# Kernel tuning notes

Hardware: AMD Instinct MI355X
Metric: run time of the kernel (lower is better)

Reference implementation:

```python
import jax, jax.numpy as jnp
import numpy as np

W_LOSS = 10.0
THRESHOLD = 1.0
ACOS_EPS = 1e-7


def _normalize(v, eps=1e-8):
    n = jnp.linalg.norm(v, axis=-1, keepdims=True)
    return v / jnp.maximum(n, eps)


def quat_to_rotmat(q):
    # q: (..., 4) in (w, x, y, z) order, as in Zhou et al. / EPN repo
    q = _normalize(q)
    w, x, y, z = q[..., 0], q[..., 1], q[..., 2], q[..., 3]
    R = jnp.stack([
        1 - 2 * (y * y + z * z), 2 * (x * y - z * w), 2 * (x * z + y * w),
        2 * (x * y + z * w), 1 - 2 * (x * x + z * z), 2 * (y * z - x * w),
        2 * (x * z - y * w), 2 * (y * z + x * w), 1 - 2 * (x * x + y * y),
    ], axis=-1)
    return R.reshape(q.shape[:-1] + (3, 3))


def acos_safe(x):
    return jnp.arccos(jnp.clip(x, -1.0 + ACOS_EPS, 1.0 - ACOS_EPS))


def angle_from_R(R):
    # R: (..., 3, 3) -> geodesic angle via trace
    tr = jnp.trace(R, axis1=-2, axis2=-1)
    return acos_safe(0.5 * (tr - 1.0))


def setup_inputs() -> dict:
    key = jax.random.key(0)
    k1, k2, k3, k4, k5 = jax.random.split(key, 5)
    B, NA, NR = 32768, 60, 4
    wts = jax.random.normal(k1, (B, NA), dtype=jnp.float32)
    label = jax.random.randint(k2, (B,), 0, NA, dtype=jnp.int64)
    y = jax.random.normal(k3, (B, NR, NA), dtype=jnp.float32)
    # gt_R and anchors are valid rotation matrices (via random quaternions)
    gt_R = quat_to_rotmat(jax.random.normal(k4, (B, NA, 4), dtype=jnp.float32))
    anchors = quat_to_rotmat(jax.random.normal(k5, (NA, 4), dtype=jnp.float32))
    return {"wts": wts, "label": label, "y": y, "gt_R": gt_R, "anchors": anchors}


def reference(wts, label, y, gt_R, anchors):
    b, na = wts.shape
    nr = y.shape[1]
    true_R = gt_R[:, 29]  # (b, 3, 3)

    # --- CrossEntropyLoss branch (classifier) ---
    logp = jax.nn.log_softmax(wts, axis=1)
    cls_loss = -jnp.mean(jnp.take_along_axis(logp, label[:, None], axis=1))
    preds = jnp.argmax(wts, axis=1)  # (b,)
    r_acc = jnp.mean((preds == label).astype(jnp.float32))

    # --- anchor-wise predicted rotations ---
    # y (b, nr, na) -> (b, na, nr) -> (b, na, 3, 3)
    pred_RAnchor = quat_to_rotmat(jnp.swapaxes(y, 1, 2))

    gt_bias = angle_from_R(gt_R)  # (b, na)
    mask = (gt_bias < THRESHOLD).astype(gt_R.dtype)[:, :, None, None]
    l2_loss = jnp.sum(jnp.square(gt_R * mask - pred_RAnchor * mask))
    loss = cls_loss + W_LOSS * l2_loss

    # --- final predicted rotation: gather best anchor, compose with anchor rot ---
    sel = jnp.take_along_axis(pred_RAnchor, preds[:, None, None, None], axis=1)[:, 0]  # (b,3,3)
    pred_R = jnp.einsum('bij,bjk->bik', anchors[preds], sel)

    # --- mean angular error ---
    ang_err = angle_from_R(jnp.einsum('bij,bkj->bik', pred_R, true_R))  # (b,)

    return (loss, cls_loss, W_LOSS * l2_loss, r_acc, ang_err)
```

## Files before the change

kernel.cpp:

```cpp
#include <hip/hip_runtime.h>
#include <math.h>

constexpr int Bc  = 32768;
constexpr int NAc = 60;

constexpr int BPB  = 4;
constexpr int NBLK = Bc / BPB;
constexpr int ROWF = NAc * 9;
constexpr int STG4 = BPB * ROWF / 4;

#define COS_ONE 0.5403023058681398f

__global__ __launch_bounds__(256) void mtl_all(
    const float* __restrict__ wts,
    const int*   __restrict__ label,
    const float* __restrict__ y,
    const float* __restrict__ gt_R,
    const float* __restrict__ anchors,
    float*       __restrict__ out,
    float*       __restrict__ l2p,
    float*       __restrict__ lpp,
    float*       __restrict__ crp)
{
    __shared__ __align__(16) float sg[BPB * ROWF + 16];
    const int tid  = threadIdx.x;
    const int lane = tid & 63;
    const int wave = tid >> 6;
    const int b0   = blockIdx.x * BPB;
    const int b    = b0 + wave;

    const float4* gb4 = (const float4*)(gt_R + (size_t)b0 * ROWF);
    float4* sg4 = (float4*)sg;
    sg4[tid]       = gb4[tid];
    sg4[tid + 256] = gb4[tid + 256];
    if (tid < STG4 - 512) sg4[tid + 512] = gb4[tid + 512];

    const int a = lane;
    int lab = label[b];
    float w = -INFINITY;
    float qw = 0, qx = 0, qy = 0, qz = 0;
    float A0=0,A1=0,A2=0,A3=0,A4=0,A5=0,A6=0,A7=0,A8=0;
    if (a < NAc) {
        w = wts[(size_t)b * NAc + a];
        const float* yb = y + (size_t)b * (4 * NAc) + a;
        qw = yb[0 * NAc];
        qx = yb[1 * NAc];
        qy = yb[2 * NAc];
        qz = yb[3 * NAc];
        const float* Ar = anchors + a * 9;
        A0 = Ar[0]; A1 = Ar[1]; A2 = Ar[2];
        A3 = Ar[3]; A4 = Ar[4]; A5 = Ar[5];
        A6 = Ar[6]; A7 = Ar[7]; A8 = Ar[8];
    }

    float n   = sqrtf(qw*qw + qx*qx + qy*qy + qz*qz);
    float inv = 1.0f / fmaxf(n, 1e-8f);
    float pw = qw*inv, px = qx*inv, py = qy*inv, pz = qz*inv;
    float R00 = 1.0f - 2.0f*(py*py + pz*pz);
    float R01 = 2.0f*(px*py - pz*pw);
    float R02 = 2.0f*(px*pz + py*pw);
    float R10 = 2.0f*(px*py + pz*pw);
    float R11 = 1.0f - 2.0f*(px*px + pz*pz);
    float R12 = 2.0f*(py*pz - px*pw);
    float R20 = 2.0f*(px*pz - py*pw);
    float R21 = 2.0f*(py*pz + px*pw);
    float R22 = 1.0f - 2.0f*(px*px + py*py);

    __syncthreads();

    float acc = 0.0f;
    if (a < NAc) {
        const float* g = sg + wave * ROWF + a * 9;
        float g0 = g[0], g1 = g[1], g2 = g[2];
        float g3 = g[3], g4 = g[4], g5 = g[5];
        float g6 = g[6], g7 = g[7], g8 = g[8];
        float xb = 0.5f * (g0 + g4 + g8 - 1.0f);
        if (xb > COS_ONE) {
            float d0 = g0-R00, d1 = g1-R01, d2 = g2-R02;
            float d3 = g3-R10, d4 = g4-R11, d5 = g5-R12;
            float d6 = g6-R20, d7 = g7-R21, d8 = g8-R22;
            acc = d0*d0 + d1*d1 + d2*d2
                + d3*d3 + d4*d4 + d5*d5
                + d6*d6 + d7*d7 + d8*d8;
        }
    }

    float mv = w;
    int   mi = lane;
    for (int off = 32; off; off >>= 1) {
        float ov = __shfl_xor(mv, off, 64);
        int   oi = __shfl_xor(mi, off, 64);
        if (ov > mv || (ov == mv && oi < mi)) { mv = ov; mi = oi; }
    }
    float e  = (a < NAc) ? expf(w - mv) : 0.0f;
    float se = e;
    for (int off = 32; off; off >>= 1) se += __shfl_xor(se, off, 64);
    float lse  = mv + logf(se);
    float wlab = __shfl(w, lab, 64);

    if (lane == mi) {
        float P00 = A0*R00 + A1*R10 + A2*R20;
        float P01 = A0*R01 + A1*R11 + A2*R21;
        float P02 = A0*R02 + A1*R12 + A2*R22;
        float P10 = A3*R00 + A4*R10 + A5*R20;
        float P11 = A3*R01 + A4*R11 + A5*R21;
        float P12 = A3*R02 + A4*R12 + A5*R22;
        float P20 = A6*R00 + A7*R10 + A8*R20;
        float P21 = A6*R01 + A7*R11 + A8*R21;
        float P22 = A6*R02 + A7*R12 + A8*R22;
        const float* tR = sg + wave * ROWF + 29 * 9;
        float tr = P00*tR[0] + P01*tR[1] + P02*tR[2]
                 + P10*tR[3] + P11*tR[4] + P12*tR[5]
                 + P20*tR[6] + P21*tR[7] + P22*tR[8];
        float cx = 0.5f * (tr - 1.0f);
        cx = fminf(fmaxf(cx, -1.0f + 1e-7f), 1.0f - 1e-7f);
        out[4 + b] = acosf(cx);
    }

    for (int off = 32; off; off >>= 1) acc += __shfl_xor(acc, off, 64);

    float* s_l2 = sg + BPB * ROWF;
    float* s_lp = s_l2 + 4;
    float* s_cr = s_lp + 4;
    if (lane == 0) {
        s_l2[wave] = acc;
        s_lp[wave] = wlab - lse;
        s_cr[wave] = (mi == lab) ? 1.0f : 0.0f;
    }
    __syncthreads();
    if (tid == 0) {
        l2p[blockIdx.x] = s_l2[0] + s_l2[1] + s_l2[2] + s_l2[3];
        lpp[blockIdx.x] = s_lp[0] + s_lp[1] + s_lp[2] + s_lp[3];
        crp[blockIdx.x] = s_cr[0] + s_cr[1] + s_cr[2] + s_cr[3];
    }
}

__global__ __launch_bounds__(256) void mtl_final(
    const float* __restrict__ l2p,
    const float* __restrict__ lpp,
    const float* __restrict__ crp,
    float*       __restrict__ out)
{
    const int tid  = threadIdx.x;
    const int lane = tid & 63;
    const int wave = tid >> 6;

    double l2 = 0.0, lp = 0.0, cr = 0.0;
    const float4* l2p4 = (const float4*)l2p;
    const float4* lpp4 = (const float4*)lpp;
    const float4* crp4 = (const float4*)crp;
    for (int i = tid; i < NBLK / 4; i += 256) {
        float4 v = l2p4[i];
        l2 += (double)v.x + (double)v.y + (double)v.z + (double)v.w;
        float4 u = lpp4[i];
        lp += (double)u.x + (double)u.y + (double)u.z + (double)u.w;
        float4 c = crp4[i];
        cr += (double)c.x + (double)c.y + (double)c.z + (double)c.w;
    }

    for (int off = 32; off; off >>= 1) {
        l2 += __shfl_xor(l2, off, 64);
        lp += __shfl_xor(lp, off, 64);
        cr += __shfl_xor(cr, off, 64);
    }
    __shared__ double s_l2[4], s_lp[4], s_cr[4];
    if (lane == 0) { s_l2[wave] = l2; s_lp[wave] = lp; s_cr[wave] = cr; }
    __syncthreads();
    if (tid == 0) {
        double t2 = s_l2[0] + s_l2[1] + s_l2[2] + s_l2[3];
        double tp = s_lp[0] + s_lp[1] + s_lp[2] + s_lp[3];
        double tc = s_cr[0] + s_cr[1] + s_cr[2] + s_cr[3];
        float cls = (float)(-tp / (double)Bc);
        float l2s = (float)(10.0 * t2);
        out[0] = cls + l2s;
        out[1] = cls;
        out[2] = l2s;
        out[3] = (float)(tc / (double)Bc);
    }
}

extern "C" void kernel_launch(void* const* d_in, const int* in_sizes, int n_in,
                              void* d_out, int out_size, void* d_ws, size_t ws_size,
                              hipStream_t stream) {
    const float* wts     = (const float*)d_in[0];
    const int*   label   = (const int*)d_in[1];
    const float* y       = (const float*)d_in[2];
    const float* gt_R    = (const float*)d_in[3];
    const float* anchors = (const float*)d_in[4];
    float* out = (float*)d_out;

    float* l2p = (float*)d_ws;
    float* lpp = l2p + NBLK;
    float* crp = lpp + NBLK;

    mtl_all  <<<NBLK, 256, 0, stream>>>(wts, label, y, gt_R, anchors,
                                        out, l2p, lpp, crp);
    mtl_final<<<1, 256, 0, stream>>>(l2p, lpp, crp, out);
}
```

Before: 140.0 us.

## Stage gt_R per wave and drop block-level partial reduction barrier

Each wave now loads its own batch row of gt_R into a private padded shared-memory slice, and writes per-row partial sums straight to global memory. This removes the second __syncthreads and the cross-wave combine in the main kernel. The final reduction kernel grows to 1024 threads and reads four times as many partials. The first __syncthreads remains, so waves still wait on each other once. The trade-off is more global partial writes and a larger final reduction.

```diff
diff --git a/kernel.cpp b/kernel.cpp
--- a/kernel.cpp
+++ b/kernel.cpp
@@ -4,10 +4,10 @@
 constexpr int Bc  = 32768;
 constexpr int NAc = 60;
 
-constexpr int BPB  = 4;
-constexpr int NBLK = Bc / BPB;
+constexpr int WPB  = 4;
+constexpr int NBLK = Bc / WPB;
 constexpr int ROWF = NAc * 9;
-constexpr int STG4 = BPB * ROWF / 4;
+constexpr int WPAD = 544;
 
 #define COS_ONE 0.5403023058681398f
 
@@ -22,18 +22,17 @@
     float*       __restrict__ lpp,
     float*       __restrict__ crp)
 {
-    __shared__ __align__(16) float sg[BPB * ROWF + 16];
+    __shared__ __align__(16) float sg[WPB * WPAD];
     const int tid  = threadIdx.x;
     const int lane = tid & 63;
     const int wave = tid >> 6;
-    const int b0   = blockIdx.x * BPB;
-    const int b    = b0 + wave;
+    const int b    = blockIdx.x * WPB + wave;
 
-    const float4* gb4 = (const float4*)(gt_R + (size_t)b0 * ROWF);
-    float4* sg4 = (float4*)sg;
-    sg4[tid]       = gb4[tid];
-    sg4[tid + 256] = gb4[tid + 256];
-    if (tid < STG4 - 512) sg4[tid + 512] = gb4[tid + 512];
+    float4*       sgw4 = (float4*)(sg + wave * WPAD);
+    const float4* gb4  = (const float4*)(gt_R + (size_t)b * ROWF);
+    sgw4[lane]      = gb4[lane];
+    sgw4[lane + 64] = gb4[lane + 64];
+    if (lane < 7) sgw4[lane + 128] = gb4[lane + 128];
 
     const int a = lane;
     int lab = label[b];
@@ -70,7 +69,7 @@
 
     float acc = 0.0f;
     if (a < NAc) {
-        const float* g = sg + wave * ROWF + a * 9;
+        const float* g = sg + wave * WPAD + a * 9;
         float g0 = g[0], g1 = g[1], g2 = g[2];
         float g3 = g[3], g4 = g[4], g5 = g[5];
         float g6 = g[6], g7 = g[7], g8 = g[8];
@@ -108,7 +107,7 @@
         float P20 = A6*R00 + A7*R10 + A8*R20;
         float P21 = A6*R01 + A7*R11 + A8*R21;
         float P22 = A6*R02 + A7*R12 + A8*R22;
-        const float* tR = sg + wave * ROWF + 29 * 9;
+        const float* tR = sg + wave * WPAD + 29 * 9;
         float tr = P00*tR[0] + P01*tR[1] + P02*tR[2]
                  + P10*tR[3] + P11*tR[4] + P12*tR[5]
                  + P20*tR[6] + P21*tR[7] + P22*tR[8];
@@ -118,24 +117,14 @@
     }
 
     for (int off = 32; off; off >>= 1) acc += __shfl_xor(acc, off, 64);
-
-    float* s_l2 = sg + BPB * ROWF;
-    float* s_lp = s_l2 + 4;
-    float* s_cr = s_lp + 4;
     if (lane == 0) {
-        s_l2[wave] = acc;
-        s_lp[wave] = wlab - lse;
-        s_cr[wave] = (mi == lab) ? 1.0f : 0.0f;
-    }
-    __syncthreads();
-    if (tid == 0) {
-        l2p[blockIdx.x] = s_l2[0] + s_l2[1] + s_l2[2] + s_l2[3];
-        lpp[blockIdx.x] = s_lp[0] + s_lp[1] + s_lp[2] + s_lp[3];
-        crp[blockIdx.x] = s_cr[0] + s_cr[1] + s_cr[2] + s_cr[3];
+        l2p[b] = acc;
+        lpp[b] = wlab - lse;
+        crp[b] = (mi == lab) ? 1.0f : 0.0f;
     }
 }
 
-__global__ __launch_bounds__(256) void mtl_final(
+__global__ __launch_bounds__(1024) void mtl_final(
     const float* __restrict__ l2p,
     const float* __restrict__ lpp,
     const float* __restrict__ crp,
@@ -149,7 +138,7 @@
     const float4* l2p4 = (const float4*)l2p;
     const float4* lpp4 = (const float4*)lpp;
     const float4* crp4 = (const float4*)crp;
-    for (int i = tid; i < NBLK / 4; i += 256) {
+    for (int i = tid; i < Bc / 4; i += 1024) {
         float4 v = l2p4[i];
         l2 += (double)v.x + (double)v.y + (double)v.z + (double)v.w;
         float4 u = lpp4[i];
@@ -163,13 +152,12 @@
         lp += __shfl_xor(lp, off, 64);
         cr += __shfl_xor(cr, off, 64);
     }
-    __shared__ double s_l2[4], s_lp[4], s_cr[4];
+    __shared__ double s_l2[16], s_lp[16], s_cr[16];
     if (lane == 0) { s_l2[wave] = l2; s_lp[wave] = lp; s_cr[wave] = cr; }
     __syncthreads();
     if (tid == 0) {
-        double t2 = s_l2[0] + s_l2[1] + s_l2[2] + s_l2[3];
-        double tp = s_lp[0] + s_lp[1] + s_lp[2] + s_lp[3];
-        double tc = s_cr[0] + s_cr[1] + s_cr[2] + s_cr[3];
+        double t2 = 0.0, tp = 0.0, tc = 0.0;
+        for (int i = 0; i < 16; ++i) { t2 += s_l2[i]; tp += s_lp[i]; tc += s_cr[i]; }
         float cls = (float)(-tp / (double)Bc);
         float l2s = (float)(10.0 * t2);
         out[0] = cls + l2s;
@@ -190,10 +178,10 @@
     float* out = (float*)d_out;
 
     float* l2p = (float*)d_ws;
-    float* lpp = l2p + NBLK;
-    float* crp = lpp + NBLK;
+    float* lpp = l2p + Bc;
+    float* crp = lpp + Bc;
 
     mtl_all  <<<NBLK, 256, 0, stream>>>(wts, label, y, gt_R, anchors,
                                         out, l2p, lpp, crp);
-    mtl_final<<<1, 256, 0, stream>>>(l2p, lpp, crp, out);
+    mtl_final<<<1, 1024, 0, stream>>>(l2p, lpp, crp, out);
 }
```

Measured after the change: 141.5 us. No clear change (+1.1%).
